# Kernel tuning notes

Hardware: AMD Instinct MI355X
Metric: run time of the kernel (lower is better)

The kernel has to match this reference:

```python
import jax, jax.numpy as jnp
import numpy as np

D_IN = 1024
D_OUT = 1024


def setup_inputs() -> dict:
    key = jax.random.key(0)
    kx, kq, kk, kv = jax.random.split(key, 4)
    B, S = 4, 2048
    scale = 1.0 / np.sqrt(D_IN)
    return {
        "x": jax.random.normal(kx, (B, S, D_IN), dtype=jnp.float32),
        "Wq": jax.random.normal(kq, (D_IN, D_OUT), dtype=jnp.float32) * scale,
        "Wk": jax.random.normal(kk, (D_IN, D_OUT), dtype=jnp.float32) * scale,
        "Wv": jax.random.normal(kv, (D_IN, D_OUT), dtype=jnp.float32) * scale,
    }


def reference(x, Wq, Wk, Wv):
    # x: [B, S, D_in]; single-head causal attention (dropout=0 -> identity)
    q = jnp.einsum("bsd,de->bse", x, Wq)
    k = jnp.einsum("bsd,de->bse", x, Wk)
    v = jnp.einsum("bsd,de->bse", x, Wv)
    S = x.shape[1]
    d_k = k.shape[-1]
    scores = jnp.einsum("bqe,bke->bqk", q, k) / jnp.sqrt(jnp.float32(d_k))
    causal = jnp.tril(jnp.ones((S, S), dtype=bool))  # True = keep
    scores = jnp.where(causal, scores, -jnp.inf)
    weights = jax.nn.softmax(scores, axis=-1)
    return jnp.einsum("bqk,bke->bqe", weights, v)
```

## Files before the change

### kernel.cpp

```cpp
#include <hip/hip_runtime.h>

typedef unsigned short u16;
typedef __bf16 bf16x8_v __attribute__((ext_vector_type(8)));
typedef float f32x4 __attribute__((ext_vector_type(4)));

__device__ __forceinline__ u16 f2bf(float f) {
    unsigned u = __float_as_uint(f);
    unsigned r = u + 0x7fffu + ((u >> 16) & 1u);
    return (u16)(r >> 16);
}
__device__ __forceinline__ float bf2f(u16 h) {
    return __uint_as_float(((unsigned)h) << 16);
}

__device__ __forceinline__ void gll16(const u16* g, u16* l) {
    __builtin_amdgcn_global_load_lds(
        (const __attribute__((address_space(1))) void*)g,
        (__attribute__((address_space(3))) void*)l, 16, 0, 0);
}

#define EXP_SHIFT 12.0f

__global__ __launch_bounds__(256) void k_cvt_x(const float* __restrict__ x,
                                               u16* __restrict__ y, int n) {
    int i = (blockIdx.x * 256 + threadIdx.x) * 8;
    if (i < n) {
        float4 a = *(const float4*)(x + i);
        float4 b = *(const float4*)(x + i + 4);
        union { int4 p; u16 h[8]; } o;
        o.h[0] = f2bf(a.x); o.h[1] = f2bf(a.y); o.h[2] = f2bf(a.z); o.h[3] = f2bf(a.w);
        o.h[4] = f2bf(b.x); o.h[5] = f2bf(b.y); o.h[6] = f2bf(b.z); o.h[7] = f2bf(b.w);
        *(int4*)(y + i) = o.p;
    }
}

__global__ __launch_bounds__(256) void k_cvt_w3(const float* __restrict__ Wq,
                                                const float* __restrict__ Wk,
                                                const float* __restrict__ Wv,
                                                u16* __restrict__ Wt3) {
    __shared__ float tile[32][33];
    const int z = blockIdx.z;
    const float* W = (z == 0) ? Wq : (z == 1) ? Wk : Wv;
    u16* Wt = Wt3 + (size_t)z * 1024 * 1024;
    int bx = blockIdx.x;
    int by = blockIdx.y;
    int tx = threadIdx.x & 31;
    int ty = threadIdx.x >> 5;
#pragma unroll
    for (int r = 0; r < 4; ++r)
        tile[ty + r * 8][tx] = W[(by * 32 + ty + r * 8) * 1024 + bx * 32 + tx];
    __syncthreads();
#pragma unroll
    for (int r = 0; r < 4; ++r)
        Wt[(bx * 32 + ty + r * 8) * 1024 + by * 32 + tx] =
            f2bf(tile[tx][ty + r * 8]);
}

__device__ __forceinline__ void gemm_core_nt(const u16* __restrict__ A,
                                             const u16* __restrict__ B,
                                             int lda, int ldb, int kLen,
                                             u16* smem, f32x4 acc[4][4]) {
    u16* As = smem;
    u16* Bs = smem + 128 * 64;
    const int tid = threadIdx.x;
    const int wave = tid >> 6;
    const int lane = tid & 63;
    const int rowA = tid >> 3;
    const int kcs  = (tid & 7) ^ (rowA & 7);
    const int row16 = lane & 15;
    const int quad = lane >> 4;
    const int sw = row16 & 7;
    const int wm = (wave >> 1) * 64;
    const int wn = (wave & 1) * 64;

#pragma unroll
    for (int i = 0; i < 4; ++i)
#pragma unroll
        for (int j = 0; j < 4; ++j) {
            f32x4 z = {0.f, 0.f, 0.f, 0.f};
            acc[i][j] = z;
        }

    const u16* Ag[4]; const u16* Bg[4];
    u16 *AsB[4], *BsB[4];
#pragma unroll
    for (int u = 0; u < 4; ++u) {
        Ag[u] = A + (size_t)(u * 32 + rowA) * lda + kcs * 8;
        Bg[u] = B + (size_t)(u * 32 + rowA) * ldb + kcs * 8;
        AsB[u] = As + (u * 256 + wave * 64) * 8;
        BsB[u] = Bs + (u * 256 + wave * 64) * 8;
    }

    const int ktiles = kLen >> 6;
    for (int kt = 0; kt < ktiles; ++kt) {
        __syncthreads();
#pragma unroll
        for (int u = 0; u < 4; ++u) gll16(Ag[u] + kt * 64, AsB[u]);
#pragma unroll
        for (int u = 0; u < 4; ++u) gll16(Bg[u] + kt * 64, BsB[u]);
        __syncthreads();
#pragma unroll
        for (int h = 0; h < 2; ++h) {
            bf16x8_v af[4], bfv[4];
            const int cp = (h * 4 + quad);
#pragma unroll
            for (int i = 0; i < 4; ++i)
                af[i] = *(const bf16x8_v*)(As + (wm + i * 16 + row16) * 64 +
                                           (cp ^ sw) * 8);
#pragma unroll
            for (int j = 0; j < 4; ++j)
                bfv[j] = *(const bf16x8_v*)(Bs + (wn + j * 16 + row16) * 64 +
                                            (cp ^ sw) * 8);
#pragma unroll
            for (int i = 0; i < 4; ++i)
#pragma unroll
                for (int j = 0; j < 4; ++j)
                    acc[i][j] = __builtin_amdgcn_mfma_f32_16x16x32_bf16(
                        af[i], bfv[j], acc[i][j], 0, 0, 0);
        }
    }
}

__device__ __forceinline__ void epi_bf16(const f32x4 acc[4][4], u16* smem,
                                         u16* __restrict__ g, int ldg) {
    const int tid = threadIdx.x;
    const int wave = tid >> 6, lane = tid & 63;
    const int row16 = lane & 15, quad = lane >> 4;
    u16* Ts = smem + wave * 2048;
#pragma unroll
    for (int jh = 0; jh < 2; ++jh) {
#pragma unroll
        for (int i = 0; i < 4; ++i)
#pragma unroll
            for (int jj = 0; jj < 2; ++jj) {
                const int j = jh * 2 + jj;
#pragma unroll
                for (int r = 0; r < 4; ++r)
                    Ts[(i * 16 + quad * 4 + r) * 32 + jj * 16 + row16] =
                        f2bf(acc[i][j][r]);
            }
#pragma unroll
        for (int s = 0; s < 4; ++s) {
            const int row = s * 16 + (lane >> 2);
            int4 val = *(const int4*)(Ts + row * 32 + (lane & 3) * 8);
            *(int4*)(g + (size_t)row * ldg + jh * 32 + (lane & 3) * 8) = val;
        }
    }
}

__device__ __forceinline__ void epi_vt(const f32x4 acc[4][4], u16* smem,
                                       u16* __restrict__ Vt, int m0w, int n0w) {
    const int tid = threadIdx.x;
    const int wave = tid >> 6, lane = tid & 63;
    const int row16 = lane & 15, quad = lane >> 4;
    const int b = m0w >> 11;
    const int sBase = m0w & 2047;
    u16* Ts = smem + wave * 4608;
#pragma unroll
    for (int p = 0; p < 2; ++p) {
#pragma unroll
        for (int i = 0; i < 4; ++i)
#pragma unroll
            for (int jj = 0; jj < 2; ++jj) {
                const int j = p * 2 + jj;
                union { unsigned long long d; u16 h[4]; } o;
#pragma unroll
                for (int r = 0; r < 4; ++r) o.h[r] = f2bf(acc[i][j][r]);
                *(unsigned long long*)(Ts + (jj * 16 + row16) * 72 +
                                       i * 16 + quad * 4) = o.d;
            }
#pragma unroll
        for (int rr = 0; rr < 4; ++rr) {
            const int ln = rr * 8 + (lane >> 3);
            const int ck = lane & 7;
            int4 val = *(const int4*)(Ts + ln * 72 + ck * 8);
            const int n = n0w + p * 32 + ln;
            *(int4*)(Vt + ((size_t)b * 1024 + n) * 2048 + sBase + ck * 8) = val;
        }
    }
}

__global__ __launch_bounds__(256, 3) void k_gemm_proj(const u16* __restrict__ X,
                                                      const u16* __restrict__ Wt3,
                                                      u16* __restrict__ Qb,
                                                      u16* __restrict__ Kb,
                                                      u16* __restrict__ Vt) {
    __shared__ u16 smem[18432];
    const int n0g = blockIdx.x * 128, m0 = blockIdx.y * 128;
    f32x4 acc[4][4];
    gemm_core_nt(X + (size_t)m0 * 1024, Wt3 + (size_t)n0g * 1024, 1024, 1024, 1024,
                 smem, acc);
    const int tid = threadIdx.x, wave = tid >> 6;
    const int wm = (wave >> 1) * 64, wn = (wave & 1) * 64;
    __syncthreads();
    if (n0g < 2048) {
        u16* Y = (n0g < 1024) ? Qb : Kb;
        const int n0 = n0g & 1023;
        epi_bf16(acc, smem, Y + (size_t)(m0 + wm) * 1024 + n0 + wn, 1024);
    } else {
        epi_vt(acc, smem, Vt, m0 + wm, (n0g - 2048) + wn);
    }
}

__global__ __launch_bounds__(256, 3) void k_gemm_scores(const u16* __restrict__ Q,
                                                        const u16* __restrict__ Kb,
                                                        u16* __restrict__ Sb,
                                                        float* __restrict__ Srow) {
    __shared__ u16 smem[16384];
    int t = blockIdx.x, b = blockIdx.y;
    int mt = 0;
    while ((mt + 1) * (mt + 2) / 2 <= t) ++mt;
    int nt = t - mt * (mt + 1) / 2;
    const u16* Qp = Q + (size_t)b * 2048 * 1024 + (size_t)mt * 128 * 1024;
    const u16* Kp = Kb + (size_t)b * 2048 * 1024 + (size_t)nt * 128 * 1024;
    u16* Sp = Sb + (size_t)b * 2048 * 2048;
    f32x4 acc[4][4];
    gemm_core_nt(Qp, Kp, 1024, 1024, 1024, smem, acc);
    const int tid = threadIdx.x, wave = tid >> 6, lane = tid & 63;
    const int wm = (wave >> 1) * 64, wn = (wave & 1) * 64;
    const int row16 = lane & 15, quad = lane >> 4;
    const int mBase = mt * 128 + wm;
    const int nBase = nt * 128 + wn;
    u16* Ts = smem + wave * 2048;
    float rs[4][4];
#pragma unroll
    for (int i = 0; i < 4; ++i)
#pragma unroll
        for (int r = 0; r < 4; ++r) rs[i][r] = 0.f;

    __syncthreads();
#pragma unroll
    for (int jh = 0; jh < 2; ++jh) {
#pragma unroll
        for (int i = 0; i < 4; ++i)
#pragma unroll
            for (int jj = 0; jj < 2; ++jj) {
                const int j = jh * 2 + jj;
                const int n = nBase + jh * 32 + jj * 16 + row16;
#pragma unroll
                for (int r = 0; r < 4; ++r) {
                    const int m = mBase + i * 16 + quad * 4 + r;
                    float e = 0.f;
                    if (n <= m)
                        e = __expf(acc[i][j][r] * 0.03125f - EXP_SHIFT);
                    rs[i][r] += e;
                    Ts[(i * 16 + quad * 4 + r) * 32 + jj * 16 + row16] = f2bf(e);
                }
            }
#pragma unroll
        for (int s = 0; s < 4; ++s) {
            const int row = s * 16 + (lane >> 2);
            int4 val = *(const int4*)(Ts + row * 32 + (lane & 3) * 8);
            *(int4*)(Sp + (size_t)(mBase + row) * 2048 +
                     nBase + jh * 32 + (lane & 3) * 8) = val;
        }
    }
    float* Sr = Srow + (size_t)b * 2048;
#pragma unroll
    for (int i = 0; i < 4; ++i)
#pragma unroll
        for (int r = 0; r < 4; ++r) {
            float s = rs[i][r];
#pragma unroll
            for (int off = 1; off < 16; off <<= 1) s += __shfl_xor(s, off);
            if (row16 == 0)
                atomicAdd(Sr + mBase + i * 16 + quad * 4 + r, s);
        }
}

__global__ __launch_bounds__(256, 3) void k_gemm_pv(const u16* __restrict__ P,
                                                    const u16* __restrict__ Vt,
                                                    const float* __restrict__ Srow,
                                                    float* __restrict__ O) {
    __shared__ u16 smem[16384];
    const int nt = blockIdx.x, mt = 15 - blockIdx.y, b = blockIdx.z;
    const u16* Pp = P + (size_t)b * 2048 * 2048 + (size_t)mt * 128 * 2048;
    const u16* Vp = Vt + (size_t)b * 1024 * 2048 + (size_t)nt * 128 * 2048;
    f32x4 acc[4][4];
    gemm_core_nt(Pp, Vp, 2048, 2048, (mt + 1) * 128, smem, acc);
    float* Op = O + (size_t)b * 2048 * 1024;
    const float* Sr = Srow + (size_t)b * 2048;
    const int tid = threadIdx.x, wave = tid >> 6, lane = tid & 63;
    const int wm = (wave >> 1) * 64, wn = (wave & 1) * 64;
    const int row16 = lane & 15, quad = lane >> 4;
    float inv[4][4];
#pragma unroll
    for (int i = 0; i < 4; ++i)
#pragma unroll
        for (int r = 0; r < 4; ++r)
            inv[i][r] = 1.0f / Sr[mt * 128 + wm + i * 16 + quad * 4 + r];
#pragma unroll
    for (int i = 0; i < 4; ++i)
#pragma unroll
        for (int j = 0; j < 4; ++j) {
            int m = mt * 128 + wm + i * 16 + quad * 4;
            int n = nt * 128 + wn + j * 16 + row16;
#pragma unroll
            for (int r = 0; r < 4; ++r)
                Op[(size_t)(m + r) * 1024 + n] = acc[i][j][r] * inv[i][r];
        }
}

extern "C" void kernel_launch(void* const* d_in, const int* in_sizes, int n_in,
                              void* d_out, int out_size, void* d_ws, size_t ws_size,
                              hipStream_t stream) {
    const float* x  = (const float*)d_in[0];
    const float* Wq = (const float*)d_in[1];
    const float* Wk = (const float*)d_in[2];
    const float* Wv = (const float*)d_in[3];
    float* out = (float*)d_out;
    char* ws = (char*)d_ws;

    u16* xb  = (u16*)(ws);
    u16* Wt3 = (u16*)(ws + (16u << 20));
    u16* Qb  = (u16*)(ws + (22u << 20));
    u16* Kb  = (u16*)(ws + (38u << 20));
    u16* Vt  = (u16*)(ws + (54u << 20));
    u16* Sb  = (u16*)(ws + (70u << 20));
    float* Srow = (float*)ws;

    k_cvt_x<<<4096, 256, 0, stream>>>(x, xb, 8192 * 1024);
    k_cvt_w3<<<dim3(32, 32, 3), 256, 0, stream>>>(Wq, Wk, Wv, Wt3);

    k_gemm_proj<<<dim3(24, 64), 256, 0, stream>>>(xb, Wt3, Qb, Kb, Vt);

    hipMemsetAsync(Srow, 0, 8192 * sizeof(float), stream);
    k_gemm_scores<<<dim3(136, 4), 256, 0, stream>>>(Qb, Kb, Sb, Srow);
    k_gemm_pv<<<dim3(8, 16, 4), 256, 0, stream>>>(Sb, Vt, Srow, out);
}
```

Before: 225.8 us.

## Split-K PV for long causal rows, fuse prep kernels and memset

Merges the x and weight conversion kernels and the row-sum memset into one prep kernel. That kernel also zeroes the bottom half of the output and a row-sum scratch area placed in the unused upper triangle of the score buffer. The PV GEMM now splits row tiles 8-15 into two K-halves that accumulate into the output with float atomics, which balances the triangular work across more blocks. The aim is to cut launch overhead and the tail imbalance, at the cost of atomic traffic and extra zeroing writes.

```diff
diff --git a/kernel.cpp b/kernel.cpp
--- a/kernel.cpp
+++ b/kernel.cpp
@@ -21,39 +21,66 @@
 
 #define EXP_SHIFT 12.0f
 
-__global__ __launch_bounds__(256) void k_cvt_x(const float* __restrict__ x,
-                                               u16* __restrict__ y, int n) {
-    int i = (blockIdx.x * 256 + threadIdx.x) * 8;
-    if (i < n) {
+__device__ __forceinline__ float* srow_ptr(u16* Sb, int b, int i) {
+    return (float*)((char*)Sb + (size_t)b * 8388608 +
+                    ((i >> 9) << 12) + 2048 + ((size_t)(i & 511) << 2));
+}
+
+__global__ __launch_bounds__(256) void k_prep(const float* __restrict__ x,
+                                              const float* __restrict__ Wq,
+                                              const float* __restrict__ Wk,
+                                              const float* __restrict__ Wv,
+                                              u16* __restrict__ xb,
+                                              u16* __restrict__ Wt3,
+                                              float* __restrict__ out,
+                                              u16* __restrict__ Sb) {
+    __shared__ float tile[32][33];
+    const int bid = blockIdx.x, tid = threadIdx.x;
+    if (bid < 4096) {
+        int i = (bid * 256 + tid) * 8;
         float4 a = *(const float4*)(x + i);
-        float4 b = *(const float4*)(x + i + 4);
+        float4 bb = *(const float4*)(x + i + 4);
         union { int4 p; u16 h[8]; } o;
-        o.h[0] = f2bf(a.x); o.h[1] = f2bf(a.y); o.h[2] = f2bf(a.z); o.h[3] = f2bf(a.w);
-        o.h[4] = f2bf(b.x); o.h[5] = f2bf(b.y); o.h[6] = f2bf(b.z); o.h[7] = f2bf(b.w);
-        *(int4*)(y + i) = o.p;
-    }
-}
-
-__global__ __launch_bounds__(256) void k_cvt_w3(const float* __restrict__ Wq,
-                                                const float* __restrict__ Wk,
-                                                const float* __restrict__ Wv,
-                                                u16* __restrict__ Wt3) {
-    __shared__ float tile[32][33];
-    const int z = blockIdx.z;
-    const float* W = (z == 0) ? Wq : (z == 1) ? Wk : Wv;
-    u16* Wt = Wt3 + (size_t)z * 1024 * 1024;
-    int bx = blockIdx.x;
-    int by = blockIdx.y;
-    int tx = threadIdx.x & 31;
-    int ty = threadIdx.x >> 5;
-#pragma unroll
-    for (int r = 0; r < 4; ++r)
-        tile[ty + r * 8][tx] = W[(by * 32 + ty + r * 8) * 1024 + bx * 32 + tx];
-    __syncthreads();
-#pragma unroll
-    for (int r = 0; r < 4; ++r)
-        Wt[(bx * 32 + ty + r * 8) * 1024 + by * 32 + tx] =
-            f2bf(tile[tx][ty + r * 8]);
+        o.h[0] = f2bf(a.x);  o.h[1] = f2bf(a.y);  o.h[2] = f2bf(a.z);  o.h[3] = f2bf(a.w);
+        o.h[4] = f2bf(bb.x); o.h[5] = f2bf(bb.y); o.h[6] = f2bf(bb.z); o.h[7] = f2bf(bb.w);
+        *(int4*)(xb + i) = o.p;
+    } else if (bid < 7168) {
+        const int w = bid - 4096;
+        const int z = w >> 10, rem = w & 1023;
+        const int bx = rem & 31, by = rem >> 5;
+        const float* W = (z == 0) ? Wq : (z == 1) ? Wk : Wv;
+        u16* Wt = Wt3 + (size_t)z * 1024 * 1024;
+        const int tx = tid & 31, ty = tid >> 5;
+#pragma unroll
+        for (int r = 0; r < 4; ++r)
+            tile[ty + r * 8][tx] = W[(by * 32 + ty + r * 8) * 1024 + bx * 32 + tx];
+        __syncthreads();
+#pragma unroll
+        for (int r = 0; r < 4; ++r)
+            Wt[(bx * 32 + ty + r * 8) * 1024 + by * 32 + tx] =
+                f2bf(tile[tx][ty + r * 8]);
+    } else if (bid < 8192) {
+        const int c = bid - 7168;
+        int4 z4 = {0, 0, 0, 0};
+        const int q0 = c * 1024 + tid * 4;
+#pragma unroll
+        for (int k = 0; k < 4; ++k) {
+            const int q = q0 + k;
+            const int b = q >> 18, off = q & 262143;
+            *(int4*)(out + (size_t)b * 2097152 + 1048576 + (size_t)off * 4) = z4;
+        }
+    } else {
+        const int chunk = tid >> 7;
+        const int t = tid & 127;
+#pragma unroll
+        for (int c = 0; c < 8; ++c) {
+            const int cc = c * 2 + chunk;
+            char* p = (char*)Sb + (size_t)(cc >> 2) * 8388608 +
+                      ((cc & 3) << 12) + 2048;
+            int4 z4 = {0, 0, 0, 0};
+            *(int4*)(p + t * 16) = z4;
+        }
+    }
 }
 
 __device__ __forceinline__ void gemm_core_nt(const u16* __restrict__ A,
@@ -204,8 +231,7 @@
 
 __global__ __launch_bounds__(256, 3) void k_gemm_scores(const u16* __restrict__ Q,
                                                         const u16* __restrict__ Kb,
-                                                        u16* __restrict__ Sb,
-                                                        float* __restrict__ Srow) {
+                                                        u16* __restrict__ Sb) {
     __shared__ u16 smem[16384];
     int t = blockIdx.x, b = blockIdx.y;
     int mt = 0;
@@ -255,7 +281,6 @@
                      nBase + jh * 32 + (lane & 3) * 8) = val;
         }
     }
-    float* Sr = Srow + (size_t)b * 2048;
 #pragma unroll
     for (int i = 0; i < 4; ++i)
 #pragma unroll
@@ -264,22 +289,26 @@
 #pragma unroll
             for (int off = 1; off < 16; off <<= 1) s += __shfl_xor(s, off);
             if (row16 == 0)
-                atomicAdd(Sr + mBase + i * 16 + quad * 4 + r, s);
-        }
-}
-
-__global__ __launch_bounds__(256, 3) void k_gemm_pv(const u16* __restrict__ P,
+                atomicAdd(srow_ptr((u16*)Sb, b, mBase + i * 16 + quad * 4 + r), s);
+        }
+}
+
+__global__ __launch_bounds__(256, 3) void k_gemm_pv(u16* __restrict__ P,
                                                     const u16* __restrict__ Vt,
-                                                    const float* __restrict__ Srow,
                                                     float* __restrict__ O) {
     __shared__ u16 smem[16384];
-    const int nt = blockIdx.x, mt = 15 - blockIdx.y, b = blockIdx.z;
-    const u16* Pp = P + (size_t)b * 2048 * 2048 + (size_t)mt * 128 * 2048;
-    const u16* Vp = Vt + (size_t)b * 1024 * 2048 + (size_t)nt * 128 * 2048;
+    const int nt = blockIdx.x, b = blockIdx.z;
+    const int y = blockIdx.y;
+    int mt, c;
+    if (y < 16) { mt = 8 + (y >> 1); c = y & 1; }
+    else        { mt = y - 16;       c = 0; }
+    const int kOff = c << 10;
+    const int kLen = min(((mt + 1) << 7) - kOff, 1024);
+    const u16* Pp = P + (size_t)b * 2048 * 2048 + (size_t)mt * 128 * 2048 + kOff;
+    const u16* Vp = Vt + (size_t)b * 1024 * 2048 + (size_t)nt * 128 * 2048 + kOff;
     f32x4 acc[4][4];
-    gemm_core_nt(Pp, Vp, 2048, 2048, (mt + 1) * 128, smem, acc);
+    gemm_core_nt(Pp, Vp, 2048, 2048, kLen, smem, acc);
     float* Op = O + (size_t)b * 2048 * 1024;
-    const float* Sr = Srow + (size_t)b * 2048;
     const int tid = threadIdx.x, wave = tid >> 6, lane = tid & 63;
     const int wm = (wave >> 1) * 64, wn = (wave & 1) * 64;
     const int row16 = lane & 15, quad = lane >> 4;
@@ -288,17 +317,31 @@
     for (int i = 0; i < 4; ++i)
 #pragma unroll
         for (int r = 0; r < 4; ++r)
-            inv[i][r] = 1.0f / Sr[mt * 128 + wm + i * 16 + quad * 4 + r];
-#pragma unroll
-    for (int i = 0; i < 4; ++i)
-#pragma unroll
-        for (int j = 0; j < 4; ++j) {
-            int m = mt * 128 + wm + i * 16 + quad * 4;
-            int n = nt * 128 + wn + j * 16 + row16;
-#pragma unroll
-            for (int r = 0; r < 4; ++r)
-                Op[(size_t)(m + r) * 1024 + n] = acc[i][j][r] * inv[i][r];
-        }
+            inv[i][r] = 1.0f / *srow_ptr(P, b, mt * 128 + wm + i * 16 + quad * 4 + r);
+    if (mt < 8) {
+#pragma unroll
+        for (int i = 0; i < 4; ++i)
+#pragma unroll
+            for (int j = 0; j < 4; ++j) {
+                int m = mt * 128 + wm + i * 16 + quad * 4;
+                int n = nt * 128 + wn + j * 16 + row16;
+#pragma unroll
+                for (int r = 0; r < 4; ++r)
+                    Op[(size_t)(m + r) * 1024 + n] = acc[i][j][r] * inv[i][r];
+            }
+    } else {
+#pragma unroll
+        for (int i = 0; i < 4; ++i)
+#pragma unroll
+            for (int j = 0; j < 4; ++j) {
+                int m = mt * 128 + wm + i * 16 + quad * 4;
+                int n = nt * 128 + wn + j * 16 + row16;
+#pragma unroll
+                for (int r = 0; r < 4; ++r)
+                    atomicAdd(&Op[(size_t)(m + r) * 1024 + n],
+                              acc[i][j][r] * inv[i][r]);
+            }
+    }
 }
 
 extern "C" void kernel_launch(void* const* d_in, const int* in_sizes, int n_in,
@@ -317,14 +360,9 @@
     u16* Kb  = (u16*)(ws + (38u << 20));
     u16* Vt  = (u16*)(ws + (54u << 20));
     u16* Sb  = (u16*)(ws + (70u << 20));
-    float* Srow = (float*)ws;
-
-    k_cvt_x<<<4096, 256, 0, stream>>>(x, xb, 8192 * 1024);
-    k_cvt_w3<<<dim3(32, 32, 3), 256, 0, stream>>>(Wq, Wk, Wv, Wt3);
-
+
+    k_prep<<<8193, 256, 0, stream>>>(x, Wq, Wk, Wv, xb, Wt3, out, Sb);
     k_gemm_proj<<<dim3(24, 64), 256, 0, stream>>>(xb, Wt3, Qb, Kb, Vt);
-
-    hipMemsetAsync(Srow, 0, 8192 * sizeof(float), stream);
-    k_gemm_scores<<<dim3(136, 4), 256, 0, stream>>>(Qb, Kb, Sb, Srow);
-    k_gemm_pv<<<dim3(8, 16, 4), 256, 0, stream>>>(Sb, Vt, Srow, out);
-}
+    k_gemm_scores<<<dim3(136, 4), 256, 0, stream>>>(Qb, Kb, Sb);
+    k_gemm_pv<<<dim3(8, 24, 4), 256, 0, stream>>>(Sb, Vt, out);
+}
```

Result: slower. 238.6 us (+5.7%).
